# Optimization experiments

Hardware: AMD Instinct MI355X
Metric: run time of the kernel (lower is better)

The kernel has to match this reference:

```python
import jax, jax.numpy as jnp
import numpy as np


def _rosa(x):
    """Suffix-automaton next-symbol predictor, faithful port of rosa() from RWKV-LM.
    x: Python list of ints (binary alphabet 0/1). Returns list y of ints in {-1,0,1}.
    """
    n = len(x)
    y = [-1] * n
    s = 2 * n + 1
    b = [None] * s   # transitions (dict per state)
    c = [-1] * s     # suffix links
    d = [0] * s      # lengths
    e = [-1] * s     # last end-position seen for the state
    b[0] = {}
    g = 0
    z = 1
    for i, t in enumerate(x):
        r = z; z += 1
        b[r] = {}
        d[r] = d[g] + 1
        p = g
        while p != -1 and t not in b[p]:
            b[p][t] = r
            p = c[p]
        if p == -1:
            c[r] = 0
        else:
            q = b[p][t]
            if d[p] + 1 == d[q]:
                c[r] = q
            else:
                u = z; z += 1
                b[u] = b[q].copy()
                d[u] = d[p] + 1
                c[u] = c[q]
                e[u] = e[q]
                while p != -1 and b[p][t] == q:
                    b[p][t] = u
                    p = c[p]
                c[q] = c[r] = u
        v = g = r
        a = -1
        while v != -1:
            if d[v] > 0 and e[v] >= 0:
                a = x[e[v] + 1]
                break
            v = c[v]
        y[i] = a
        v = g
        while v != -1 and e[v] < i:
            e[v] = i
            v = c[v]
    return y


def _rosa_idx(x):
    """Host-side construction of idx[B,T,C] from float input x (bits = x>0).
    The suffix automaton is inherently sequential / data-dependent per (b,c)
    sequence, exactly as in the original module."""
    bits = (np.asarray(x) > 0).astype(np.int64)  # [B,T,C]
    B, T, C = bits.shape
    idx = np.empty((B, T, C), dtype=np.int64)
    for bb in range(B):
        for cc in range(C):
            idx[bb, :, cc] = _rosa(bits[bb, :, cc].tolist())
    return idx


def setup_inputs() -> dict:
    key = jax.random.key(0)
    k1, k2, k3 = jax.random.split(key, 3)
    B, T, C = 2, 2048, 128
    x = jax.random.normal(k1, (B, T, C), dtype=jnp.float32)
    # parameters init'd at +/-1e-5 in the module; use tiny random values of the
    # same scale so the two tables are distinguishable in correctness checks.
    emb0 = jax.random.normal(k2, (1, 1, C), dtype=jnp.float32) * 1e-5
    emb1 = jax.random.normal(k3, (1, 1, C), dtype=jnp.float32) * 1e-5
    return {"x": x, "emb0": emb0, "emb1": emb1}


def reference(x, emb0, emb1):
    # idx in {-1, 0, 1}: predicted next bit after the longest matched suffix
    idx = jnp.asarray(_rosa_idx(x))  # [B,T,C] int64
    e0 = jnp.broadcast_to(emb0, x.shape)
    e1 = jnp.broadcast_to(emb1, x.shape)
    out = jnp.where(idx == -1, jnp.zeros_like(x), jnp.where(idx == 1, e1, e0))
    return out
```

## Files before the change

kernel.cpp:

```cpp
#include <hip/hip_runtime.h>


#define B_   2
#define T_   2048
#define C_   128
#define MAXS 4100

typedef unsigned int       u32;
typedef unsigned short     u16;
typedef unsigned long long u64;
typedef u16 __attribute__((may_alias)) u16a;
typedef u32 __attribute__((may_alias)) u32a;

__global__ __launch_bounds__(64)
void rosa_kernel(const float* __restrict__ x,
                 const float* __restrict__ emb0,
                 const float* __restrict__ emb1,
                 float* __restrict__ out)
{
    __shared__ u64 st[MAXS];
    __shared__ u64 bits[T_ / 64];
    __shared__ signed char y8[T_];
    __shared__ u32 scratch[64];

    const int blk  = blockIdx.x;
    const int bb   = blk >> 7;
    const int cc   = blk & (C_ - 1);
    const int lane = threadIdx.x;

    const float* xp = x + (size_t)bb * T_ * C_ + cc;
    for (int k = 0; k < T_ / 64; ++k) {
        float v = xp[(size_t)(k * 64 + lane) * C_];
        u64 m = __ballot(v > 0.0f);
        if (lane == 0) bits[k] = m;
    }
    __syncthreads();

    u16a* tr16 = (u16a*)st;
    u32a* st32 = (u32a*)st;

    u64 curw = bits[0];
    {
        const int t0 = (int)(curw & 1ull);
        const int f0 = (int)((curw >> 1) & 1ull);
        if (lane == 0) {
            u32 tr0 = 0xFFFFFFFFu & ~(0xFFFFu << (t0 * 16));
            tr0 |= (1u << (t0 * 16));
            st[0] = ((u64)((u32)((0 | (f0 << 15)) << 16)) << 32) | tr0;
            st[1] = ((u64)((u32)((1 | (f0 << 15)) << 16)) << 32) | 0xFFFFFFFFu;
            y8[0] = (signed char)(-1);
        }
    }

    bool act  = (lane == 63);
    int  vid  = 0;
    int  vlen = 0;
    int  g    = 1;
    int  z    = 2;
    u64  nxtw = bits[1];
    u32  trv  = st32[2 * vid];

    for (int i = 1; i < T_; ++i) {
        if ((i & 63) == 0) { curw = nxtw; int w = (i >> 6) + 1; nxtw = (w < T_/64) ? bits[w] : 0ull; }
        const int ii = i & 63;
        const int t  = (int)((curw >> ii) & 1ull);
        const int fb = (ii == 63) ? (int)(nxtw & 1ull) : (int)((curw >> (ii + 1)) & 1ull);
        const int sh = t << 4;

        const int qj = act ? (int)((trv >> sh) & 0xFFFFu) : 0xFFFF;
        const u64 hasmask = __ballot(qj != 0xFFFF);
        const bool found  = hasmask != 0ull;
        const int  k      = found ? (int)__builtin_ctzll(hasmask) : 64;
        const int  ks     = k & 63;

        const int qe  = (qj == 0xFFFF) ? 0 : qj;
        const u64 stq = st[qe];
        const u64 Am  = __ballot(act);
        const u64 below = Am & ((1ull << lane) - 1ull);
        const int pidx  = below ? (63 - __builtin_clzll(below)) : 0;
        const int prevq = __builtin_amdgcn_ds_bpermute(pidx << 2, qj);

        const u32 trq = (u32)(stq & 0xFFFFFFFFu);
        const u32 elq = (u32)(stq >> 32);
        const int lenq = (int)((elq >> 16) & 0x7FFFu);

        const int q      = __builtin_amdgcn_readlane(qj, ks);
        const int lenp   = __builtin_amdgcn_readlane(vlen, ks);
        const int lenq_k = __builtin_amdgcn_readlane(lenq, ks);
        const u32 elq_k  = (u32)__builtin_amdgcn_readlane((int)elq, ks);

        const bool clone = found && (lenp + 1 != lenq_k);
        const int r  = z;
        const int u_ = z + 1;
        z += clone ? 2 : 1;

        const u64 aliasm = __ballot(act && lane < k && vid == q);
        const bool qstale = (q == g) || (aliasm != 0ull);

        const u64 aboveK = ~((2ull << ks) - 1ull);
        const u64 eqm  = __ballot(qj == q);
        const u64 badm = Am & ~eqm & aboveK;
        const int b0   = badm ? (int)__builtin_ctzll(badm) : 64;
        const bool redir = clone && act && lane >= k && lane < b0 && (qj == q);

        const bool keep = act && lane >= k && (lane == k || qj != prevq);
        const int id_cand  = (clone && lane == k) ? u_ : qj;
        const int len_cand = (clone && lane == k) ? (lenp + 1) : lenq;
        const u64 keepm = __ballot(keep);

        if (act && lane < k) tr16[4 * vid + t] = (u16)r;
        if (lane == 0)       tr16[4 * g + t]   = (u16)r;
        if (redir)           tr16[4 * vid + t] = (u16)u_;
        if (clone && lane == 0) {
            u32 trqk = (u32)__builtin_amdgcn_readlane((int)trq, ks);
            if (qstale) trqk = (trqk & ~(0xFFFFu << sh)) | ((u32)r << sh);
            const u32 w1u = (u32)(u16)i | ((u32)((lenp + 1) | (fb << 15)) << 16);
            st[u_] = ((u64)w1u << 32) | trqk;
        }

        const u32 efv = (u32)(u16)i | ((u32)(len_cand | (fb << 15)) << 16);
        if (keep) st32[2 * id_cand + 1] = efv;
        if (lane == 0) {
            const u32 w1r = (u32)(u16)i | ((u32)((i + 1) | (fb << 15)) << 16);
            st[r] = ((u64)w1r << 32) | 0xFFFFFFFFu;
            st32[1] = (u32)(u16)i | ((u32)(0 | (fb << 15)) << 16);
            const int a = found ? (int)((elq_k >> 31) & 1u) : -1;
            y8[i] = (signed char)a;
        }

        const bool k63 = (keepm >> 63) & 1ull;
        const u64  kmid = keepm & 0x7FFFFFFFFFFFFFFFull;
        const int  P = kmid ? (63 - __builtin_clzll(kmid)) : 0;
        const int  newpos = P + 1;
        const bool recomp = k63 && (newpos >= 63);

        bool actn = (keep && lane < 63) || (lane == 63);
        int  idn  = (keep && lane < 63) ? id_cand : 0;
        int  lenn = (keep && lane < 63) ? len_cand : 0;

        if (k63 && !recomp) {
            const int sId  = __builtin_amdgcn_readlane(id_cand, 63);
            const int sLen = __builtin_amdgcn_readlane(len_cand, 63);
            if (lane == newpos) { idn = sId; lenn = sLen; actn = true; }
        }
        if (recomp) {
            const int dest = 1 + (int)__builtin_popcountll(keepm & ((1ull << lane) - 1ull));
            if (keep) scratch[dest] = (u32)id_cand | ((u32)len_cand << 16);
            const int cnt = (int)__builtin_popcountll(keepm);
            const u32 sc = scratch[lane];
            const bool inr = (lane >= 1 && lane <= cnt);
            actn = inr || (lane == 63);
            idn  = (lane == 63) ? 0 : (inr ? (int)(sc & 0xFFFFu) : 0);
            lenn = (lane == 63) ? 0 : (inr ? (int)(sc >> 16) : 0);
        }

        act = actn; vid = idn; vlen = lenn; g = r;
        trv = st32[2 * vid];
    }
    __syncthreads();

    const float e0 = emb0[cc];
    const float e1 = emb1[cc];
    float* op = out + (size_t)bb * T_ * C_ + cc;
    for (int tt = lane; tt < T_; tt += 64) {
        int yv = y8[tt];
        op[(size_t)tt * C_] = (yv < 0) ? 0.0f : (yv ? e1 : e0);
    }
}

extern "C" void kernel_launch(void* const* d_in, const int* in_sizes, int n_in,
                              void* d_out, int out_size, void* d_ws, size_t ws_size,
                              hipStream_t stream)
{
    const float* x    = (const float*)d_in[0];
    const float* emb0 = (const float*)d_in[1];
    const float* emb1 = (const float*)d_in[2];
    float* out = (float*)d_out;

    dim3 grid(B_ * C_);
    dim3 block(64);
    rosa_kernel<<<grid, block, 0, stream>>>(x, emb0, emb1, out);
}
```

Baseline: 1.073 ms.

## Carry transition words in registers with tag-based staleness instead of reloading state

```diff
diff --git a/kernel.cpp b/kernel.cpp
--- a/kernel.cpp
+++ b/kernel.cpp
@@ -19,9 +19,10 @@
                  float* __restrict__ out)
 {
     __shared__ u64 st[MAXS];
+    __shared__ u16 tag[MAXS];
     __shared__ u64 bits[T_ / 64];
-    __shared__ signed char y8[T_];
-    __shared__ u32 scratch[64];
+    __shared__ u64 y2[T_ / 32];
+    __shared__ u64 scratch[64];
 
     const int blk  = blockIdx.x;
     const int bb   = blk >> 7;
@@ -34,31 +35,28 @@
         u64 m = __ballot(v > 0.0f);
         if (lane == 0) bits[k] = m;
     }
+    for (int k = lane; k < MAXS; k += 64) tag[k] = 0xFFFFu;
     __syncthreads();
 
     u16a* tr16 = (u16a*)st;
     u32a* st32 = (u32a*)st;
 
     u64 curw = bits[0];
-    {
-        const int t0 = (int)(curw & 1ull);
-        const int f0 = (int)((curw >> 1) & 1ull);
-        if (lane == 0) {
-            u32 tr0 = 0xFFFFFFFFu & ~(0xFFFFu << (t0 * 16));
-            tr0 |= (1u << (t0 * 16));
-            st[0] = ((u64)((u32)((0 | (f0 << 15)) << 16)) << 32) | tr0;
-            st[1] = ((u64)((u32)((1 | (f0 << 15)) << 16)) << 32) | 0xFFFFFFFFu;
-            y8[0] = (signed char)(-1);
-        }
+    const int t0 = (int)(curw & 1ull);
+    const int f0 = (int)((curw >> 1) & 1ull);
+    const u32 tr0w = (0xFFFFFFFFu & ~(0xFFFFu << (t0 << 4))) | (1u << (t0 << 4));
+    if (lane == 0) {
+        st[0] = ((u64)(u32)((0 | (f0 << 15)) << 16) << 32) | tr0w;
+        st[1] = ((u64)(u32)((1 | (f0 << 15)) << 16) << 32) | 0xFFFFFFFFu;
     }
+    __syncthreads();
 
     bool act  = (lane == 63);
-    int  vid  = 0;
-    int  vlen = 0;
-    int  g    = 1;
-    int  z    = 2;
+    int  vid  = 0, vlen = 0;
+    u32  trv  = tr0w;
+    int  g = 1, z = 2;
+    u64  yacc = 0;
     u64  nxtw = bits[1];
-    u32  trv  = st32[2 * vid];
 
     for (int i = 1; i < T_; ++i) {
         if ((i & 63) == 0) { curw = nxtw; int w = (i >> 6) + 1; nxtw = (w < T_/64) ? bits[w] : 0ull; }
@@ -68,6 +66,7 @@
         const int sh = t << 4;
 
         const int qj = act ? (int)((trv >> sh) & 0xFFFFu) : 0xFFFF;
+        const u64 Am = __ballot(act);
         const u64 hasmask = __ballot(qj != 0xFFFF);
         const bool found  = hasmask != 0ull;
         const int  k      = found ? (int)__builtin_ctzll(hasmask) : 64;
@@ -75,13 +74,12 @@
 
         const int qe  = (qj == 0xFFFF) ? 0 : qj;
         const u64 stq = st[qe];
-        const u64 Am  = __ballot(act);
         const u64 below = Am & ((1ull << lane) - 1ull);
         const int pidx  = below ? (63 - __builtin_clzll(below)) : 0;
         const int prevq = __builtin_amdgcn_ds_bpermute(pidx << 2, qj);
 
-        const u32 trq = (u32)(stq & 0xFFFFFFFFu);
-        const u32 elq = (u32)(stq >> 32);
+        const u32 trq  = (u32)stq;
+        const u32 elq  = (u32)(stq >> 32);
         const int lenq = (int)((elq >> 16) & 0x7FFFu);
 
         const int q      = __builtin_amdgcn_readlane(qj, ks);
@@ -94,39 +92,49 @@
         const int u_ = z + 1;
         z += clone ? 2 : 1;
 
-        const u64 aliasm = __ballot(act && lane < k && vid == q);
-        const bool qstale = (q == g) || (aliasm != 0ull);
-
         const u64 aboveK = ~((2ull << ks) - 1ull);
         const u64 eqm  = __ballot(qj == q);
         const u64 badm = Am & ~eqm & aboveK;
         const int b0   = badm ? (int)__builtin_ctzll(badm) : 64;
+        const bool walkw = act && lane < k;
         const bool redir = clone && act && lane >= k && lane < b0 && (qj == q);
 
+        if (walkw)     { tr16[4 * vid + t] = (u16)r;  tag[vid] = (u16)((i << 1) | 0); }
+        if (lane == 0) { tr16[4 * g + t]   = (u16)r;  tag[g]   = (u16)((i << 1) | 0); }
+        if (redir)     { tr16[4 * vid + t] = (u16)u_; tag[vid] = (u16)((i << 1) | 1); }
+
         const bool keep = act && lane >= k && (lane == k || qj != prevq);
-        const int id_cand  = (clone && lane == k) ? u_ : qj;
-        const int len_cand = (clone && lane == k) ? (lenp + 1) : lenq;
+        const int id_cand  = (clone && lane == ks) ? u_ : qj;
+        const int len_cand = (clone && lane == ks) ? (lenp + 1) : lenq;
         const u64 keepm = __ballot(keep);
 
-        if (act && lane < k) tr16[4 * vid + t] = (u16)r;
-        if (lane == 0)       tr16[4 * g + t]   = (u16)r;
-        if (redir)           tr16[4 * vid + t] = (u16)u_;
-        if (clone && lane == 0) {
-            u32 trqk = (u32)__builtin_amdgcn_readlane((int)trq, ks);
-            if (qstale) trqk = (trqk & ~(0xFFFFu << sh)) | ((u32)r << sh);
-            const u32 w1u = (u32)(u16)i | ((u32)((lenp + 1) | (fb << 15)) << 16);
-            st[u_] = ((u64)w1u << 32) | trqk;
-        }
+        const int tga = act ? ((clone && lane == ks) ? q : qe) : 0;
+        const u16 tg  = tag[tga];
 
         const u32 efv = (u32)(u16)i | ((u32)(len_cand | (fb << 15)) << 16);
         if (keep) st32[2 * id_cand + 1] = efv;
         if (lane == 0) {
             const u32 w1r = (u32)(u16)i | ((u32)((i + 1) | (fb << 15)) << 16);
             st[r] = ((u64)w1r << 32) | 0xFFFFFFFFu;
-            st32[1] = (u32)(u16)i | ((u32)(0 | (fb << 15)) << 16);
-            const int a = found ? (int)((elq_k >> 31) & 1u) : -1;
-            y8[i] = (signed char)a;
         }
+
+        const int a = found ? (int)((elq_k >> 31) & 1u) : -1;
+        yacc |= (u64)(u32)(a + 1) << (2 * (i & 31));
+        if ((i & 31) == 31) { if (lane == 0) y2[i >> 5] = yacc; yacc = 0; }
+
+        const bool tvalid = ((int)(tg >> 1) == i);
+        const u32  nslot  = (tg & 1) ? (u32)u_ : (u32)r;
+        u32 trvn = trq;
+        if (tvalid) trvn = (trvn & ~(0xFFFFu << sh)) | (nslot << sh);
+
+        if (clone && lane == ks) {
+            const u32 w1u = (u32)(u16)i | ((u32)((lenp + 1) | (fb << 15)) << 16);
+            st[u_] = ((u64)w1u << 32) | trvn;
+        }
+
+        const int sId  = __builtin_amdgcn_readlane(id_cand, 63);
+        const int sLen = __builtin_amdgcn_readlane(len_cand, 63);
+        const u32 sW   = (u32)__builtin_amdgcn_readlane((int)trvn, 63);
 
         const bool k63 = (keepm >> 63) & 1ull;
         const u64  kmid = keepm & 0x7FFFFFFFFFFFFFFFull;
@@ -134,28 +142,32 @@
         const int  newpos = P + 1;
         const bool recomp = k63 && (newpos >= 63);
 
-        bool actn = (keep && lane < 63) || (lane == 63);
-        int  idn  = (keep && lane < 63) ? id_cand : 0;
-        int  lenn = (keep && lane < 63) ? len_cand : 0;
-
-        if (k63 && !recomp) {
-            const int sId  = __builtin_amdgcn_readlane(id_cand, 63);
-            const int sLen = __builtin_amdgcn_readlane(len_cand, 63);
-            if (lane == newpos) { idn = sId; lenn = sLen; actn = true; }
-        }
+        bool actn = keep && lane < 63;
+        int  idn  = actn ? id_cand : 0;
+        int  lenn = actn ? len_cand : 0;
+        u32  trvn2 = trvn;
+        if (k63 && !recomp && lane == newpos) { actn = true; idn = sId; lenn = sLen; trvn2 = sW; }
         if (recomp) {
             const int dest = 1 + (int)__builtin_popcountll(keepm & ((1ull << lane) - 1ull));
-            if (keep) scratch[dest] = (u32)id_cand | ((u32)len_cand << 16);
+            if (keep) scratch[dest] = (u64)(u16)id_cand | ((u64)(u16)len_cand << 16)
+                                    | ((u64)trvn << 32);
             const int cnt = (int)__builtin_popcountll(keepm);
-            const u32 sc = scratch[lane];
+            const u64 sc = scratch[lane];
             const bool inr = (lane >= 1 && lane <= cnt);
-            actn = inr || (lane == 63);
-            idn  = (lane == 63) ? 0 : (inr ? (int)(sc & 0xFFFFu) : 0);
-            lenn = (lane == 63) ? 0 : (inr ? (int)(sc >> 16) : 0);
+            actn = inr;
+            idn  = inr ? (int)(sc & 0xFFFFu) : 0;
+            lenn = inr ? (int)((sc >> 16) & 0xFFFFu) : 0;
+            trvn2 = inr ? (u32)(sc >> 32) : 0u;
+        }
+        if (lane == 63) {
+            actn = true; idn = 0; lenn = 0;
+            u32 rw = trv;
+            if (!found)     rw = (rw & ~(0xFFFFu << sh)) | ((u32)r  << sh);
+            else if (redir) rw = (rw & ~(0xFFFFu << sh)) | ((u32)u_ << sh);
+            trvn2 = rw;
         }
 
-        act = actn; vid = idn; vlen = lenn; g = r;
-        trv = st32[2 * vid];
+        act = actn; vid = idn; vlen = lenn; trv = trvn2; g = r;
     }
     __syncthreads();
 
@@ -163,8 +175,8 @@
     const float e1 = emb1[cc];
     float* op = out + (size_t)bb * T_ * C_ + cc;
     for (int tt = lane; tt < T_; tt += 64) {
-        int yv = y8[tt];
-        op[(size_t)tt * C_] = (yv < 0) ? 0.0f : (yv ? e1 : e0);
+        const int code = (int)((y2[tt >> 5] >> (2 * (tt & 31))) & 3ull);
+        op[(size_t)tt * C_] = (code == 0) ? 0.0f : (code == 1 ? e0 : e1);
     }
 }
 
```

New measurement: 1.317 ms. 22.7% more time.
